# Kernel tuning notes

Measured on AMD Instinct MI355X. Metric: run time of the kernel, lower is better.

The kernel has to match this reference:

```python
import jax, jax.numpy as jnp
import numpy as np

D = 1024      # hidden_size
F = 4096      # intermediate_size
E = 16        # num_experts
TOPK = 2      # num_experts_per_tok
B, L = 1, 2048


def setup_inputs() -> dict:
    key = jax.random.key(0)
    ks = jax.random.split(key, 5)
    s = 0.02
    return {
        "x": jax.random.normal(ks[0], (B, L, D), dtype=jnp.float32),
        "gate_w": jax.random.normal(ks[1], (E, D), dtype=jnp.float32) * s,
        "w1s": jax.random.normal(ks[2], (E, F, D), dtype=jnp.float32) * s,  # per-expert w1 (out,in)
        "w2s": jax.random.normal(ks[3], (E, D, F), dtype=jnp.float32) * s,  # per-expert w2
        "w3s": jax.random.normal(ks[4], (E, F, D), dtype=jnp.float32) * s,  # per-expert w3
    }


def reference(x, gate_w, w1s, w2s, w3s):
    b, l, d = x.shape
    xf = x.reshape(-1, d)                                   # [T, D]
    router_logits = xf @ gate_w.T                           # [T, E]
    topw, topi = jax.lax.top_k(router_logits.astype(jnp.float32), TOPK)
    topw = jax.nn.softmax(topw, axis=-1).astype(x.dtype)    # [T, K]
    T = xf.shape[0]
    # dense combine weights: zero for unselected experts (same math as masked loop)
    combine = jnp.zeros((T, E), x.dtype).at[jnp.arange(T)[:, None], topi].add(topw)

    def body(acc, ew):
        w1, w2, w3, cw = ew                                 # cw: [T]
        h = jax.nn.silu(xf @ w1.T) * (xf @ w3.T)            # [T, F]
        return acc + cw[:, None] * (h @ w2.T), None

    out, _ = jax.lax.scan(body, jnp.zeros_like(xf), (w1s, w2s, w3s, combine.T))
    return out.reshape(b, l, d), router_logits
```

## Files before the change

### kernel.cpp

```cpp
#include <hip/hip_runtime.h>

#define D_DIM 1024
#define F_DIM 4096
#define E_NUM 16
#define T_NUM 2048

typedef __bf16 bf16x8 __attribute__((ext_vector_type(8)));
typedef float f32x4 __attribute__((ext_vector_type(4)));

__device__ __forceinline__ unsigned pack2bf(float a, float b) {
  unsigned ua = __builtin_bit_cast(unsigned, a);
  unsigned ub = __builtin_bit_cast(unsigned, b);
  return ((ub + 0x8000u) & 0xffff0000u) | ((ua + 0x8000u) >> 16);
}
__device__ __forceinline__ unsigned short f2bf(float a) {
  unsigned ua = __builtin_bit_cast(unsigned, a);
  return (unsigned short)((ua + 0x8000u) >> 16);
}
__device__ __forceinline__ bf16x8 cvt8(f32x4 a, f32x4 b) {
  bf16x8 r;
  r[0] = (__bf16)a[0]; r[1] = (__bf16)a[1]; r[2] = (__bf16)a[2]; r[3] = (__bf16)a[3];
  r[4] = (__bf16)b[0]; r[5] = (__bf16)b[1]; r[6] = (__bf16)b[2]; r[7] = (__bf16)b[3];
  return r;
}
__device__ __forceinline__ void gload16(const void* g, void* l) {
  __builtin_amdgcn_global_load_lds(
      (const __attribute__((address_space(1))) unsigned*)g,
      (__attribute__((address_space(3))) unsigned*)l, 16, 0, 0);
}

__global__ __launch_bounds__(256) void moe_xcast(
    const float* __restrict__ x, unsigned short* __restrict__ xbf)
{
  int i = blockIdx.x * 256 + threadIdx.x;
  const f32x4* p = (const f32x4*)x + (size_t)i * 2;
  f32x4 a = p[0], b = p[1];
  uint4 o;
  o.x = pack2bf(a[0], a[1]); o.y = pack2bf(a[2], a[3]);
  o.z = pack2bf(b[0], b[1]); o.w = pack2bf(b[2], b[3]);
  ((uint4*)xbf)[i] = o;
}

__global__ __launch_bounds__(256) void moe_router(
    const float* __restrict__ x, const float* __restrict__ gate,
    float* __restrict__ logits_out, int* __restrict__ topi, float* __restrict__ topw)
{
  __shared__ float lg[16][17];
  int tid = threadIdx.x;
  int tbase = blockIdx.x * 16;
  int tt = tid >> 4, e = tid & 15;
  const float4* xr = (const float4*)(x + (size_t)(tbase + tt) * D_DIM);
  const float4* gw = (const float4*)(gate + (size_t)e * D_DIM);
  float acc = 0.f;
  #pragma unroll 4
  for (int k = 0; k < D_DIM / 4; ++k) {
    float4 a = xr[k], b = gw[k];
    acc += a.x * b.x + a.y * b.y + a.z * b.z + a.w * b.w;
  }
  lg[tt][e] = acc;
  logits_out[(size_t)(tbase + tt) * E_NUM + e] = acc;
  __syncthreads();
  if (tid < 16) {
    int t = tid;
    float best = -1e30f; int i0 = 0;
    #pragma unroll
    for (int j = 0; j < 16; ++j) { float v = lg[t][j]; if (v > best) { best = v; i0 = j; } }
    float best1 = -1e30f; int i1 = 0;
    #pragma unroll
    for (int j = 0; j < 16; ++j) { if (j == i0) continue; float v = lg[t][j]; if (v > best1) { best1 = v; i1 = j; } }
    float e1 = __expf(best1 - best);
    float inv = 1.f / (1.f + e1);
    int gt = tbase + t;
    topi[gt * 2]     = i0;  topi[gt * 2 + 1] = i1;
    topw[gt * 2]     = inv; topw[gt * 2 + 1] = e1 * inv;
  }
}

__global__ __launch_bounds__(1024) void moe_route_build(
    const int* __restrict__ topi,
    int* __restrict__ cnt, int* __restrict__ rowbase,
    int* __restrict__ rowlist, int* __restrict__ rowpos)
{
  __shared__ int scnt[16];
  __shared__ int sbase[17];
  int wave = threadIdx.x >> 6;
  int lane = threadIdx.x & 63;
  int total = 0;
  for (int c = 0; c < (T_NUM * 2) / 64; ++c) {
    int s = c * 64 + lane;
    unsigned long long m = __ballot(topi[s] == wave);
    total += __popcll(m);
  }
  if (lane == 0) scnt[wave] = total;
  __syncthreads();
  if (threadIdx.x == 0) {
    int acc = 0;
    for (int e2 = 0; e2 < 16; ++e2) { sbase[e2] = acc; cnt[e2] = scnt[e2]; acc += scnt[e2]; }
    sbase[16] = acc;
    for (int e2 = 0; e2 <= 16; ++e2) rowbase[e2] = sbase[e2];
  }
  __syncthreads();
  int running = sbase[wave];
  for (int c = 0; c < (T_NUM * 2) / 64; ++c) {
    int s = c * 64 + lane;
    int ei = topi[s];
    unsigned long long m = __ballot(ei == wave);
    if (ei == wave) {
      int pos = running + __popcll(m & ((1ull << lane) - 1ull));
      rowlist[pos] = s;
      rowpos[s] = pos;
    }
    running += __popcll(m);
  }
}

__global__ __launch_bounds__(512, 2) void moe_gemm1(
    const unsigned short* __restrict__ xbf, const float* __restrict__ w1s, const float* __restrict__ w3s,
    const int* __restrict__ cnt, const int* __restrict__ rowbase, const int* __restrict__ rowlist,
    unsigned short* __restrict__ H)
{
  int nt = blockIdx.x, mt = blockIdx.y, e = blockIdx.z;
  int Ne = cnt[e];
  if (mt * 320 >= Ne) return;
  int rbase = rowbase[e];

  __shared__ char smem[107520];

  int tid = threadIdx.x, lane = tid & 63, wave = tid >> 6;

  const float* w1e = w1s + (size_t)e * F_DIM * D_DIM + (size_t)(nt * 128) * D_DIM;
  const float* w3e = w3s + (size_t)e * F_DIM * D_DIM + (size_t)(nt * 128) * D_DIM;
  const char* p1[2]; const char* p3[2];
  #pragma unroll
  for (int it = 0; it < 2; ++it) {
    int r = (wave * 2 + it) * 8 + (lane >> 3);
    int c = (lane & 7) ^ (r & 7);
    p1[it] = (const char*)(w1e + (size_t)r * D_DIM) + c * 16;
    p3[it] = (const char*)(w3e + (size_t)r * D_DIM) + c * 16;
  }

  const char* px[3];
  unsigned xdoff[3];
  #pragma unroll
  for (int it = 0; it < 3; ++it) {
    int ch = wave + it * 8;
    if (ch < 20) {
      int r = ch * 16 + (lane >> 2);
      int lr = mt * 320 + r;
      int tok = (lr < Ne) ? (rowlist[rbase + lr] >> 1) : 0;
      int c = (lane & 3) ^ ((r >> 1) & 3);
      px[it] = (const char*)(xbf + (size_t)tok * D_DIM) + c * 16;
      xdoff[it] = (unsigned)(ch * 1024 + lane * 16);
    } else {
      px[it] = (const char*)xbf + (lane & 3) * 16;
      xdoff[it] = 0xFFFFFFFFu;
    }
  }

  int wm = wave >> 1, wn = wave & 1;
  int lr16 = lane & 15, lq = lane >> 4;

  unsigned offA[5];
  #pragma unroll
  for (int mi = 0; mi < 5; ++mi) {
    int m = wm * 80 + mi * 16 + lr16;
    offA[mi] = (unsigned)(m * 64 + ((lq ^ ((m >> 1) & 3)) * 16));
  }
  unsigned offB[4][2];
  #pragma unroll
  for (int ni = 0; ni < 4; ++ni) {
    int n = wn * 64 + ni * 16 + lr16;
    #pragma unroll
    for (int h = 0; h < 2; ++h)
      offB[ni][h] = (unsigned)(n * 128 + (((lq * 2 + h) ^ (n & 7)) * 16));
  }

  unsigned wdst = (unsigned)((wave * 2) * 1024 + lane * 16);

  f32x4 acc1[5][4], acc3[5][4];
  #pragma unroll
  for (int i = 0; i < 5; ++i)
    #pragma unroll
    for (int j = 0; j < 4; ++j) { acc1[i][j] = {0.f,0.f,0.f,0.f}; acc3[i][j] = {0.f,0.f,0.f,0.f}; }

  auto STAGE = [&](unsigned bsel, int ks) {
    #pragma unroll
    for (int it = 0; it < 3; ++it) {
      char* dst = (xdoff[it] == 0xFFFFFFFFu)
                    ? (smem + 106496 + lane * 16)
                    : (smem + bsel * 20480u + xdoff[it]);
      gload16(px[it] + ks * 64, dst);
    }
    #pragma unroll
    for (int it = 0; it < 2; ++it) {
      gload16(p1[it] + ks * 128, smem + 40960 + bsel * 16384u + wdst + it * 1024);
      gload16(p3[it] + ks * 128, smem + 73728 + bsel * 16384u + wdst + it * 1024);
    }
  };

  STAGE(0, 0);
  unsigned buf = 0;
  for (int ks = 0; ks < 32; ++ks) {
    if (ks < 31) {
      STAGE(buf ^ 1u, ks + 1);
      asm volatile("s_waitcnt vmcnt(7)" ::: "memory");
    } else {
      asm volatile("s_waitcnt vmcnt(0)" ::: "memory");
    }
    __builtin_amdgcn_s_barrier();
    unsigned xb = buf * 20480u;
    unsigned w1b = 40960 + buf * 16384u;
    unsigned w3b = 73728 + buf * 16384u;
    bf16x8 af[5];
    #pragma unroll
    for (int mi = 0; mi < 5; ++mi)
      af[mi] = *(const bf16x8*)(smem + xb + offA[mi]);
    #pragma unroll
    for (int ni = 0; ni < 4; ++ni) {
      bf16x8 b1 = cvt8(*(const f32x4*)(smem + w1b + offB[ni][0]),
                       *(const f32x4*)(smem + w1b + offB[ni][1]));
      bf16x8 b3 = cvt8(*(const f32x4*)(smem + w3b + offB[ni][0]),
                       *(const f32x4*)(smem + w3b + offB[ni][1]));
      #pragma unroll
      for (int mi = 0; mi < 5; ++mi) {
        acc1[mi][ni] = __builtin_amdgcn_mfma_f32_16x16x32_bf16(af[mi], b1, acc1[mi][ni], 0, 0, 0);
        acc3[mi][ni] = __builtin_amdgcn_mfma_f32_16x16x32_bf16(af[mi], b3, acc3[mi][ni], 0, 0, 0);
      }
    }
    __builtin_amdgcn_s_barrier();
    buf ^= 1u;
  }

  #pragma unroll
  for (int mi = 0; mi < 5; ++mi) {
    int mb = wm * 80 + mi * 16 + lq * 4;
    #pragma unroll
    for (int r = 0; r < 4; ++r) {
      int lrow = mt * 320 + mb + r;
      if (lrow < Ne) {
        size_t hrow = (size_t)(rbase + lrow) * F_DIM;
        #pragma unroll
        for (int ni = 0; ni < 4; ++ni) {
          int f = nt * 128 + wn * 64 + ni * 16 + lr16;
          float a1v = acc1[mi][ni][r];
          float a3v = acc3[mi][ni][r];
          float hv = (a1v / (1.f + __expf(-a1v))) * a3v;
          H[hrow + f] = f2bf(hv);
        }
      }
    }
  }
}

__global__ __launch_bounds__(512, 2) void moe_gemm2(
    const unsigned short* __restrict__ H, const float* __restrict__ w2s,
    const int* __restrict__ cnt, const int* __restrict__ rowbase,
    unsigned short* __restrict__ Ybf)
{
  int nt = blockIdx.x, mt = blockIdx.y, e = blockIdx.z;
  int Ne = cnt[e];
  if (mt * 320 >= Ne) return;
  int rbase = rowbase[e];

  __shared__ char smem[114688];

  int tid = threadIdx.x, lane = tid & 63, wave = tid >> 6;

  const float* w2e = w2s + (size_t)e * D_DIM * F_DIM + (size_t)(nt * 64) * F_DIM;
  const char* pb[2];
  #pragma unroll
  for (int it = 0; it < 2; ++it) {
    int r = (wave * 2 + it) * 4 + (lane >> 4);
    int c = (lane & 15) ^ (r & 7);
    pb[it] = (const char*)(w2e + (size_t)r * F_DIM) + c * 16;
  }

  const char* pa[5];
  unsigned adoff[5];
  #pragma unroll
  for (int it = 0; it < 5; ++it) {
    int ch = wave + it * 8;
    int r = ch * 8 + (lane >> 3);
    int grow = mt * 320 + r; if (grow >= Ne) grow = Ne - 1;
    int c = (lane & 7) ^ (r & 7);
    pa[it] = (const char*)(H + (size_t)(rbase + grow) * F_DIM) + c * 16;
    adoff[it] = (unsigned)(ch * 1024 + lane * 16);
  }

  int wm = wave >> 1, wn = wave & 1;
  int lr16 = lane & 15, lq = lane >> 4;

  unsigned dstB = (unsigned)((wave * 2) * 1024 + lane * 16);

  f32x4 acc[5][2];
  #pragma unroll
  for (int i = 0; i < 5; ++i) { acc[i][0] = {0.f,0.f,0.f,0.f}; acc[i][1] = {0.f,0.f,0.f,0.f}; }

  auto STAGE = [&](unsigned bsel, int ks) {
    #pragma unroll
    for (int it = 0; it < 5; ++it)
      gload16(pa[it] + ks * 128, smem + bsel * 40960u + adoff[it]);
    #pragma unroll
    for (int it = 0; it < 2; ++it)
      gload16(pb[it] + ks * 256, smem + 81920 + bsel * 16384u + dstB + it * 1024);
  };

  STAGE(0, 0);
  unsigned buf = 0;
  for (int ks = 0; ks < 64; ++ks) {
    if (ks < 63) {
      STAGE(buf ^ 1u, ks + 1);
      asm volatile("s_waitcnt vmcnt(7)" ::: "memory");
    } else {
      asm volatile("s_waitcnt vmcnt(0)" ::: "memory");
    }
    __builtin_amdgcn_s_barrier();
    unsigned ab = buf * 40960u;
    unsigned bb = 81920 + buf * 16384u;
    #pragma unroll
    for (int ksub = 0; ksub < 2; ++ksub) {
      bf16x8 bfr[2];
      #pragma unroll
      for (int ni = 0; ni < 2; ++ni) {
        int n = wn * 32 + ni * 16 + lr16;
        unsigned o0 = (unsigned)(n * 256 + (((ksub * 8 + lq * 2 + 0) ^ (n & 7)) * 16));
        unsigned o1 = (unsigned)(n * 256 + (((ksub * 8 + lq * 2 + 1) ^ (n & 7)) * 16));
        bfr[ni] = cvt8(*(const f32x4*)(smem + bb + o0), *(const f32x4*)(smem + bb + o1));
      }
      #pragma unroll
      for (int mi = 0; mi < 5; ++mi) {
        int m = wm * 80 + mi * 16 + lr16;
        unsigned off = (unsigned)(m * 128 + (((ksub * 4 + lq) ^ (m & 7)) * 16));
        bf16x8 af = *(const bf16x8*)(smem + ab + off);
        #pragma unroll
        for (int ni = 0; ni < 2; ++ni)
          acc[mi][ni] = __builtin_amdgcn_mfma_f32_16x16x32_bf16(af, bfr[ni], acc[mi][ni], 0, 0, 0);
      }
    }
    __builtin_amdgcn_s_barrier();
    buf ^= 1u;
  }

  #pragma unroll
  for (int mi = 0; mi < 5; ++mi) {
    int mb = wm * 80 + mi * 16 + lq * 4;
    #pragma unroll
    for (int r = 0; r < 4; ++r) {
      int lrow = mt * 320 + mb + r;
      if (lrow < Ne) {
        size_t yrow = (size_t)(rbase + lrow) * D_DIM;
        #pragma unroll
        for (int ni = 0; ni < 2; ++ni) {
          int d = nt * 64 + wn * 32 + ni * 16 + lr16;
          Ybf[yrow + d] = f2bf(acc[mi][ni][r]);
        }
      }
    }
  }
}

__global__ __launch_bounds__(128) void moe_combine(
    const unsigned short* __restrict__ Ybf, const int* __restrict__ rowpos,
    const float* __restrict__ topw, float* __restrict__ out)
{
  int t = blockIdx.x, tid = threadIdx.x;
  int r0 = rowpos[t * 2], r1 = rowpos[t * 2 + 1];
  float p0 = topw[t * 2], p1 = topw[t * 2 + 1];
  uint4 a = ((const uint4*)(Ybf + (size_t)r0 * D_DIM))[tid];
  uint4 b = ((const uint4*)(Ybf + (size_t)r1 * D_DIM))[tid];
  float4 o0, o1;
  #define LO(u) __builtin_bit_cast(float, (unsigned)((u) << 16))
  #define HI(u) __builtin_bit_cast(float, (unsigned)((u) & 0xffff0000u))
  o0.x = p0 * LO(a.x) + p1 * LO(b.x);  o0.y = p0 * HI(a.x) + p1 * HI(b.x);
  o0.z = p0 * LO(a.y) + p1 * LO(b.y);  o0.w = p0 * HI(a.y) + p1 * HI(b.y);
  o1.x = p0 * LO(a.z) + p1 * LO(b.z);  o1.y = p0 * HI(a.z) + p1 * HI(b.z);
  o1.z = p0 * LO(a.w) + p1 * LO(b.w);  o1.w = p0 * HI(a.w) + p1 * HI(b.w);
  #undef LO
  #undef HI
  float4* orow = (float4*)(out + (size_t)t * D_DIM);
  orow[tid * 2]     = o0;
  orow[tid * 2 + 1] = o1;
}

extern "C" void kernel_launch(void* const* d_in, const int* in_sizes, int n_in,
                              void* d_out, int out_size, void* d_ws, size_t ws_size,
                              hipStream_t stream) {
  const float* x    = (const float*)d_in[0];
  const float* gate = (const float*)d_in[1];
  const float* w1   = (const float*)d_in[2];
  const float* w2   = (const float*)d_in[3];
  const float* w3   = (const float*)d_in[4];
  float* out    = (float*)d_out;
  float* logits = out + (size_t)T_NUM * D_DIM;

  char* ws = (char*)d_ws;
  int*   cnt     = (int*)(ws + 0);
  int*   rowbase = (int*)(ws + 64);
  int*   topi    = (int*)(ws + 1024);
  float* topw    = (float*)(ws + 1024 + 16384);
  int*   rowlist = (int*)(ws + 1024 + 32768);
  int*   rowpos  = (int*)(ws + 1024 + 49152);
  unsigned short* H   = (unsigned short*)(ws + 131072);
  unsigned short* Ybf = (unsigned short*)(ws + 131072 + 33554432);
  unsigned short* xbf = (unsigned short*)(ws + 131072 + 33554432 + 8388608);

  moe_xcast<<<(T_NUM * D_DIM) / (256 * 8), 256, 0, stream>>>(x, xbf);
  moe_router<<<T_NUM / 16, 256, 0, stream>>>(x, gate, logits, topi, topw);
  moe_route_build<<<1, 1024, 0, stream>>>(topi, cnt, rowbase, rowlist, rowpos);
  moe_gemm1<<<dim3(32, 4, 16), 512, 0, stream>>>(xbf, w1, w3, cnt, rowbase, rowlist, H);
  moe_gemm2<<<dim3(16, 4, 16), 512, 0, stream>>>(H, w2, cnt, rowbase, Ybf);
  moe_combine<<<T_NUM, 128, 0, stream>>>(Ybf, rowpos, topw, out);
}
```

Baseline: 344.4 us.

## Split MoE GEMM work across 1024-thread blocks, halving per-wave accumulators

Both expert GEMM kernels move from 512 to 1024 threads per block. In gemm1, one wave group computes the w1 projection and the other computes w3, so each wave keeps half the accumulators. The SiLU·w3 product is formed by passing the silu(w1) values through shared memory in four bands with extra barriers. In gemm2 each wave owns a single 16-wide N fragment. The grid's M dimension grows to 13 tiles so experts holding more than 1280 routed rows are covered. The aim is lower register pressure and more waves to hide latency, at the cost of extra barrier-serialised epilogue passes and one block per CU.

```diff
diff --git a/kernel.cpp b/kernel.cpp
--- a/kernel.cpp
+++ b/kernel.cpp
@@ -114,7 +114,7 @@
   }
 }
 
-__global__ __launch_bounds__(512, 2) void moe_gemm1(
+__global__ __launch_bounds__(1024, 1) void moe_gemm1(
     const unsigned short* __restrict__ xbf, const float* __restrict__ w1s, const float* __restrict__ w3s,
     const int* __restrict__ cnt, const int* __restrict__ rowbase, const int* __restrict__ rowlist,
     unsigned short* __restrict__ H)
@@ -124,40 +124,39 @@
   if (mt * 320 >= Ne) return;
   int rbase = rowbase[e];
 
-  __shared__ char smem[107520];
+  __shared__ char smem[106496];
 
   int tid = threadIdx.x, lane = tid & 63, wave = tid >> 6;
+
+  int nx = (wave < 4) ? 2 : 1;
+  const char* px[2];
+  unsigned xoff[2];
+  #pragma unroll
+  for (int it = 0; it < 2; ++it) {
+    int ch = wave + it * 16;
+    if (ch < 20) {
+      int row = ch * 16 + (lane >> 2);
+      int lr = mt * 320 + row;
+      int tok = (lr < Ne) ? (rowlist[rbase + lr] >> 1) : 0;
+      int c4 = (lane & 3) ^ ((row >> 1) & 3);
+      px[it] = (const char*)(xbf + (size_t)tok * D_DIM) + c4 * 16;
+      xoff[it] = (unsigned)(ch * 1024 + lane * 16);
+    } else {
+      px[it] = (const char*)xbf;
+      xoff[it] = 0;
+    }
+  }
 
   const float* w1e = w1s + (size_t)e * F_DIM * D_DIM + (size_t)(nt * 128) * D_DIM;
   const float* w3e = w3s + (size_t)e * F_DIM * D_DIM + (size_t)(nt * 128) * D_DIM;
-  const char* p1[2]; const char* p3[2];
-  #pragma unroll
-  for (int it = 0; it < 2; ++it) {
-    int r = (wave * 2 + it) * 8 + (lane >> 3);
-    int c = (lane & 7) ^ (r & 7);
-    p1[it] = (const char*)(w1e + (size_t)r * D_DIM) + c * 16;
-    p3[it] = (const char*)(w3e + (size_t)r * D_DIM) + c * 16;
-  }
-
-  const char* px[3];
-  unsigned xdoff[3];
-  #pragma unroll
-  for (int it = 0; it < 3; ++it) {
-    int ch = wave + it * 8;
-    if (ch < 20) {
-      int r = ch * 16 + (lane >> 2);
-      int lr = mt * 320 + r;
-      int tok = (lr < Ne) ? (rowlist[rbase + lr] >> 1) : 0;
-      int c = (lane & 3) ^ ((r >> 1) & 3);
-      px[it] = (const char*)(xbf + (size_t)tok * D_DIM) + c * 16;
-      xdoff[it] = (unsigned)(ch * 1024 + lane * 16);
-    } else {
-      px[it] = (const char*)xbf + (lane & 3) * 16;
-      xdoff[it] = 0xFFFFFFFFu;
-    }
-  }
-
-  int wm = wave >> 1, wn = wave & 1;
+  int rw = wave * 8 + (lane >> 3);
+  int cw = (lane & 7) ^ (rw & 7);
+  const char* pw1 = (const char*)(w1e + (size_t)rw * D_DIM) + cw * 16;
+  const char* pw3 = (const char*)(w3e + (size_t)rw * D_DIM) + cw * 16;
+  unsigned woff = (unsigned)(wave * 1024 + lane * 16);
+
+  int wgrp = wave >> 3, wl = wave & 7;
+  int wm = wl >> 1, wn = wl & 1;
   int lr16 = lane & 15, lq = lane >> 4;
 
   unsigned offA[5];
@@ -168,34 +167,25 @@
   }
   unsigned offB[4][2];
   #pragma unroll
-  for (int ni = 0; ni < 4; ++ni) {
-    int n = wn * 64 + ni * 16 + lr16;
+  for (int nf = 0; nf < 4; ++nf) {
+    int n = wn * 64 + nf * 16 + lr16;
     #pragma unroll
     for (int h = 0; h < 2; ++h)
-      offB[ni][h] = (unsigned)(n * 128 + (((lq * 2 + h) ^ (n & 7)) * 16));
-  }
-
-  unsigned wdst = (unsigned)((wave * 2) * 1024 + lane * 16);
-
-  f32x4 acc1[5][4], acc3[5][4];
+      offB[nf][h] = (unsigned)(n * 128 + (((lq * 2 + h) ^ (n & 7)) * 16));
+  }
+  unsigned wbase0 = wgrp ? 73728u : 40960u;
+
+  f32x4 acc[5][4];
   #pragma unroll
   for (int i = 0; i < 5; ++i)
     #pragma unroll
-    for (int j = 0; j < 4; ++j) { acc1[i][j] = {0.f,0.f,0.f,0.f}; acc3[i][j] = {0.f,0.f,0.f,0.f}; }
+    for (int j = 0; j < 4; ++j) acc[i][j] = {0.f, 0.f, 0.f, 0.f};
 
   auto STAGE = [&](unsigned bsel, int ks) {
-    #pragma unroll
-    for (int it = 0; it < 3; ++it) {
-      char* dst = (xdoff[it] == 0xFFFFFFFFu)
-                    ? (smem + 106496 + lane * 16)
-                    : (smem + bsel * 20480u + xdoff[it]);
-      gload16(px[it] + ks * 64, dst);
-    }
-    #pragma unroll
-    for (int it = 0; it < 2; ++it) {
-      gload16(p1[it] + ks * 128, smem + 40960 + bsel * 16384u + wdst + it * 1024);
-      gload16(p3[it] + ks * 128, smem + 73728 + bsel * 16384u + wdst + it * 1024);
-    }
+    gload16(px[0] + ks * 64, smem + bsel * 20480u + xoff[0]);
+    if (nx == 2) gload16(px[1] + ks * 64, smem + bsel * 20480u + xoff[1]);
+    gload16(pw1 + ks * 128, smem + 40960 + bsel * 16384u + woff);
+    gload16(pw3 + ks * 128, smem + 73728 + bsel * 16384u + woff);
   };
 
   STAGE(0, 0);
@@ -203,56 +193,72 @@
   for (int ks = 0; ks < 32; ++ks) {
     if (ks < 31) {
       STAGE(buf ^ 1u, ks + 1);
-      asm volatile("s_waitcnt vmcnt(7)" ::: "memory");
+      if (wave < 4) asm volatile("s_waitcnt vmcnt(4)" ::: "memory");
+      else          asm volatile("s_waitcnt vmcnt(3)" ::: "memory");
     } else {
       asm volatile("s_waitcnt vmcnt(0)" ::: "memory");
     }
     __builtin_amdgcn_s_barrier();
     unsigned xb = buf * 20480u;
-    unsigned w1b = 40960 + buf * 16384u;
-    unsigned w3b = 73728 + buf * 16384u;
-    bf16x8 af[5];
-    #pragma unroll
-    for (int mi = 0; mi < 5; ++mi)
-      af[mi] = *(const bf16x8*)(smem + xb + offA[mi]);
-    #pragma unroll
-    for (int ni = 0; ni < 4; ++ni) {
-      bf16x8 b1 = cvt8(*(const f32x4*)(smem + w1b + offB[ni][0]),
-                       *(const f32x4*)(smem + w1b + offB[ni][1]));
-      bf16x8 b3 = cvt8(*(const f32x4*)(smem + w3b + offB[ni][0]),
-                       *(const f32x4*)(smem + w3b + offB[ni][1]));
+    unsigned wb = wbase0 + buf * 16384u;
+    bf16x8 bfr[4];
+    #pragma unroll
+    for (int nf = 0; nf < 4; ++nf)
+      bfr[nf] = cvt8(*(const f32x4*)(smem + wb + offB[nf][0]),
+                     *(const f32x4*)(smem + wb + offB[nf][1]));
+    #pragma unroll
+    for (int mi = 0; mi < 5; ++mi) {
+      bf16x8 af = *(const bf16x8*)(smem + xb + offA[mi]);
+      #pragma unroll
+      for (int nf = 0; nf < 4; ++nf)
+        acc[mi][nf] = __builtin_amdgcn_mfma_f32_16x16x32_bf16(af, bfr[nf], acc[mi][nf], 0, 0, 0);
+    }
+    __builtin_amdgcn_s_barrier();
+    buf ^= 1u;
+  }
+
+  float* xch = (float*)smem;
+  for (int band = 0; band < 4; ++band) {
+    if (wgrp == 0 && wm == band) {
       #pragma unroll
       for (int mi = 0; mi < 5; ++mi) {
-        acc1[mi][ni] = __builtin_amdgcn_mfma_f32_16x16x32_bf16(af[mi], b1, acc1[mi][ni], 0, 0, 0);
-        acc3[mi][ni] = __builtin_amdgcn_mfma_f32_16x16x32_bf16(af[mi], b3, acc3[mi][ni], 0, 0, 0);
-      }
-    }
-    __builtin_amdgcn_s_barrier();
-    buf ^= 1u;
-  }
-
-  #pragma unroll
-  for (int mi = 0; mi < 5; ++mi) {
-    int mb = wm * 80 + mi * 16 + lq * 4;
-    #pragma unroll
-    for (int r = 0; r < 4; ++r) {
-      int lrow = mt * 320 + mb + r;
-      if (lrow < Ne) {
-        size_t hrow = (size_t)(rbase + lrow) * F_DIM;
         #pragma unroll
-        for (int ni = 0; ni < 4; ++ni) {
-          int f = nt * 128 + wn * 64 + ni * 16 + lr16;
-          float a1v = acc1[mi][ni][r];
-          float a3v = acc3[mi][ni][r];
-          float hv = (a1v / (1.f + __expf(-a1v))) * a3v;
-          H[hrow + f] = f2bf(hv);
+        for (int r = 0; r < 4; ++r) {
+          int rb = mi * 16 + lq * 4 + r;
+          #pragma unroll
+          for (int nf = 0; nf < 4; ++nf) {
+            int col = wn * 64 + nf * 16 + lr16;
+            float a = acc[mi][nf][r];
+            xch[rb * 132 + col] = a / (1.f + __expf(-a));
+          }
         }
       }
     }
-  }
-}
-
-__global__ __launch_bounds__(512, 2) void moe_gemm2(
+    asm volatile("s_waitcnt lgkmcnt(0)" ::: "memory");
+    __builtin_amdgcn_s_barrier();
+    if (wgrp == 1 && wm == band) {
+      #pragma unroll
+      for (int mi = 0; mi < 5; ++mi) {
+        #pragma unroll
+        for (int r = 0; r < 4; ++r) {
+          int rb = mi * 16 + lq * 4 + r;
+          int lrow = mt * 320 + band * 80 + rb;
+          if (lrow < Ne) {
+            size_t hrow = (size_t)(rbase + lrow) * F_DIM;
+            #pragma unroll
+            for (int nf = 0; nf < 4; ++nf) {
+              int col = wn * 64 + nf * 16 + lr16;
+              H[hrow + nt * 128 + col] = f2bf(xch[rb * 132 + col] * acc[mi][nf][r]);
+            }
+          }
+        }
+      }
+    }
+    __builtin_amdgcn_s_barrier();
+  }
+}
+
+__global__ __launch_bounds__(1024, 1) void moe_gemm2(
     const unsigned short* __restrict__ H, const float* __restrict__ w2s,
     const int* __restrict__ cnt, const int* __restrict__ rowbase,
     unsigned short* __restrict__ Ybf)
@@ -266,43 +272,43 @@
 
   int tid = threadIdx.x, lane = tid & 63, wave = tid >> 6;
 
+  int na = (wave < 8) ? 3 : 2;
+  const char* pa[3];
+  unsigned aoff[3];
+  #pragma unroll
+  for (int it = 0; it < 3; ++it) {
+    int ch = wave + it * 16;
+    if (ch < 40) {
+      int row = ch * 8 + (lane >> 3);
+      int grow = mt * 320 + row; if (grow >= Ne) grow = Ne - 1;
+      int c8 = (lane & 7) ^ (row & 7);
+      pa[it] = (const char*)(H + (size_t)(rbase + grow) * F_DIM) + c8 * 16;
+      aoff[it] = (unsigned)(ch * 1024 + lane * 16);
+    } else {
+      pa[it] = (const char*)H;
+      aoff[it] = 0;
+    }
+  }
+
   const float* w2e = w2s + (size_t)e * D_DIM * F_DIM + (size_t)(nt * 64) * F_DIM;
-  const char* pb[2];
-  #pragma unroll
-  for (int it = 0; it < 2; ++it) {
-    int r = (wave * 2 + it) * 4 + (lane >> 4);
-    int c = (lane & 15) ^ (r & 7);
-    pb[it] = (const char*)(w2e + (size_t)r * F_DIM) + c * 16;
-  }
-
-  const char* pa[5];
-  unsigned adoff[5];
-  #pragma unroll
-  for (int it = 0; it < 5; ++it) {
-    int ch = wave + it * 8;
-    int r = ch * 8 + (lane >> 3);
-    int grow = mt * 320 + r; if (grow >= Ne) grow = Ne - 1;
-    int c = (lane & 7) ^ (r & 7);
-    pa[it] = (const char*)(H + (size_t)(rbase + grow) * F_DIM) + c * 16;
-    adoff[it] = (unsigned)(ch * 1024 + lane * 16);
-  }
-
-  int wm = wave >> 1, wn = wave & 1;
+  int rw = wave * 4 + (lane >> 4);
+  int cw = (lane & 15) ^ (rw & 7);
+  const char* pw2 = (const char*)(w2e + (size_t)rw * F_DIM) + cw * 16;
+  unsigned woff = (unsigned)(wave * 1024 + lane * 16);
+
+  int wm = wave >> 2, wn = wave & 3;
   int lr16 = lane & 15, lq = lane >> 4;
-
-  unsigned dstB = (unsigned)((wave * 2) * 1024 + lane * 16);
-
-  f32x4 acc[5][2];
-  #pragma unroll
-  for (int i = 0; i < 5; ++i) { acc[i][0] = {0.f,0.f,0.f,0.f}; acc[i][1] = {0.f,0.f,0.f,0.f}; }
+  int n = wn * 16 + lr16;
+
+  f32x4 acc[5];
+  #pragma unroll
+  for (int i = 0; i < 5; ++i) acc[i] = {0.f, 0.f, 0.f, 0.f};
 
   auto STAGE = [&](unsigned bsel, int ks) {
-    #pragma unroll
-    for (int it = 0; it < 5; ++it)
-      gload16(pa[it] + ks * 128, smem + bsel * 40960u + adoff[it]);
-    #pragma unroll
-    for (int it = 0; it < 2; ++it)
-      gload16(pb[it] + ks * 256, smem + 81920 + bsel * 16384u + dstB + it * 1024);
+    gload16(pa[0] + ks * 128, smem + bsel * 40960u + aoff[0]);
+    gload16(pa[1] + ks * 128, smem + bsel * 40960u + aoff[1]);
+    if (na == 3) gload16(pa[2] + ks * 128, smem + bsel * 40960u + aoff[2]);
+    gload16(pw2 + ks * 256, smem + 81920 + bsel * 16384u + woff);
   };
 
   STAGE(0, 0);
@@ -310,7 +316,8 @@
   for (int ks = 0; ks < 64; ++ks) {
     if (ks < 63) {
       STAGE(buf ^ 1u, ks + 1);
-      asm volatile("s_waitcnt vmcnt(7)" ::: "memory");
+      if (wave < 8) asm volatile("s_waitcnt vmcnt(4)" ::: "memory");
+      else          asm volatile("s_waitcnt vmcnt(3)" ::: "memory");
     } else {
       asm volatile("s_waitcnt vmcnt(0)" ::: "memory");
     }
@@ -319,22 +326,15 @@
     unsigned bb = 81920 + buf * 16384u;
     #pragma unroll
     for (int ksub = 0; ksub < 2; ++ksub) {
-      bf16x8 bfr[2];
-      #pragma unroll
-      for (int ni = 0; ni < 2; ++ni) {
-        int n = wn * 32 + ni * 16 + lr16;
-        unsigned o0 = (unsigned)(n * 256 + (((ksub * 8 + lq * 2 + 0) ^ (n & 7)) * 16));
-        unsigned o1 = (unsigned)(n * 256 + (((ksub * 8 + lq * 2 + 1) ^ (n & 7)) * 16));
-        bfr[ni] = cvt8(*(const f32x4*)(smem + bb + o0), *(const f32x4*)(smem + bb + o1));
-      }
+      unsigned o0 = (unsigned)(n * 256 + (((ksub * 8 + lq * 2 + 0) ^ (n & 7)) * 16));
+      unsigned o1 = (unsigned)(n * 256 + (((ksub * 8 + lq * 2 + 1) ^ (n & 7)) * 16));
+      bf16x8 bfr = cvt8(*(const f32x4*)(smem + bb + o0), *(const f32x4*)(smem + bb + o1));
       #pragma unroll
       for (int mi = 0; mi < 5; ++mi) {
         int m = wm * 80 + mi * 16 + lr16;
         unsigned off = (unsigned)(m * 128 + (((ksub * 4 + lq) ^ (m & 7)) * 16));
         bf16x8 af = *(const bf16x8*)(smem + ab + off);
-        #pragma unroll
-        for (int ni = 0; ni < 2; ++ni)
-          acc[mi][ni] = __builtin_amdgcn_mfma_f32_16x16x32_bf16(af, bfr[ni], acc[mi][ni], 0, 0, 0);
+        acc[mi] = __builtin_amdgcn_mfma_f32_16x16x32_bf16(af, bfr, acc[mi], 0, 0, 0);
       }
     }
     __builtin_amdgcn_s_barrier();
@@ -349,11 +349,7 @@
       int lrow = mt * 320 + mb + r;
       if (lrow < Ne) {
         size_t yrow = (size_t)(rbase + lrow) * D_DIM;
-        #pragma unroll
-        for (int ni = 0; ni < 2; ++ni) {
-          int d = nt * 64 + wn * 32 + ni * 16 + lr16;
-          Ybf[yrow + d] = f2bf(acc[mi][ni][r]);
-        }
+        Ybf[yrow + nt * 64 + n] = f2bf(acc[mi][r]);
       }
     }
   }
@@ -407,7 +403,7 @@
   moe_xcast<<<(T_NUM * D_DIM) / (256 * 8), 256, 0, stream>>>(x, xbf);
   moe_router<<<T_NUM / 16, 256, 0, stream>>>(x, gate, logits, topi, topw);
   moe_route_build<<<1, 1024, 0, stream>>>(topi, cnt, rowbase, rowlist, rowpos);
-  moe_gemm1<<<dim3(32, 4, 16), 512, 0, stream>>>(xbf, w1, w3, cnt, rowbase, rowlist, H);
-  moe_gemm2<<<dim3(16, 4, 16), 512, 0, stream>>>(H, w2, cnt, rowbase, Ybf);
+  moe_gemm1<<<dim3(32, 13, 16), 1024, 0, stream>>>(xbf, w1, w3, cnt, rowbase, rowlist, H);
+  moe_gemm2<<<dim3(16, 13, 16), 1024, 0, stream>>>(H, w2, cnt, rowbase, Ybf);
   moe_combine<<<T_NUM, 128, 0, stream>>>(Ybf, rowpos, topw, out);
 }
```

Result: slower. 470.7 us (+36.7%).

## Pre-gather routed tokens to bf16 and widen gemm2 N tile

Applied to the files above, without the earlier changes.

A new gather kernel replaces the full-x bf16 cast and writes each routed token's row contiguously in expert order. gemm1 can then load activations with plain strided addressing instead of per-row token lookups, and it no longer needs the dummy-destination path for idle waves. gemm2 doubles its output-column tile from 64 to 128, so each H tile is reused across more columns and fewer H loads are issued. The M grid is cut to two 320-row tiles per expert, which caps each expert at 640 tokens; gemm2's larger LDS footprint may also reduce occupancy.

```diff
diff --git a/kernel.cpp b/kernel.cpp
--- a/kernel.cpp
+++ b/kernel.cpp
@@ -27,18 +27,6 @@
   __builtin_amdgcn_global_load_lds(
       (const __attribute__((address_space(1))) unsigned*)g,
       (__attribute__((address_space(3))) unsigned*)l, 16, 0, 0);
-}
-
-__global__ __launch_bounds__(256) void moe_xcast(
-    const float* __restrict__ x, unsigned short* __restrict__ xbf)
-{
-  int i = blockIdx.x * 256 + threadIdx.x;
-  const f32x4* p = (const f32x4*)x + (size_t)i * 2;
-  f32x4 a = p[0], b = p[1];
-  uint4 o;
-  o.x = pack2bf(a[0], a[1]); o.y = pack2bf(a[2], a[3]);
-  o.z = pack2bf(b[0], b[1]); o.w = pack2bf(b[2], b[3]);
-  ((uint4*)xbf)[i] = o;
 }
 
 __global__ __launch_bounds__(256) void moe_router(
@@ -114,9 +102,21 @@
   }
 }
 
+__global__ __launch_bounds__(256) void moe_gather(
+    const float* __restrict__ x, const int* __restrict__ rowlist,
+    const int* __restrict__ rowbase, unsigned short* __restrict__ xg)
+{
+  int pos = blockIdx.x;
+  int total = rowbase[16];
+  int tok = (pos < total) ? (rowlist[pos] >> 1) : 0;
+  f32x4 v = ((const f32x4*)(x + (size_t)tok * D_DIM))[threadIdx.x];
+  ((uint2*)(xg + (size_t)pos * D_DIM))[threadIdx.x] =
+      make_uint2(pack2bf(v[0], v[1]), pack2bf(v[2], v[3]));
+}
+
 __global__ __launch_bounds__(512, 2) void moe_gemm1(
-    const unsigned short* __restrict__ xbf, const float* __restrict__ w1s, const float* __restrict__ w3s,
-    const int* __restrict__ cnt, const int* __restrict__ rowbase, const int* __restrict__ rowlist,
+    const unsigned short* __restrict__ xg, const float* __restrict__ w1s, const float* __restrict__ w3s,
+    const int* __restrict__ cnt, const int* __restrict__ rowbase,
     unsigned short* __restrict__ H)
 {
   int nt = blockIdx.x, mt = blockIdx.y, e = blockIdx.z;
@@ -124,9 +124,25 @@
   if (mt * 320 >= Ne) return;
   int rbase = rowbase[e];
 
-  __shared__ char smem[107520];
+  __shared__ char smem[106496];
 
   int tid = threadIdx.x, lane = tid & 63, wave = tid >> 6;
+
+  const char* px[3];
+  unsigned xoff[3];
+  #pragma unroll
+  for (int it = 0; it < 3; ++it) {
+    int ch = wave + it * 8;
+    if (ch < 20) {
+      int row = ch * 16 + (lane >> 2);
+      int slot = (lane & 3) ^ ((row >> 1) & 3);
+      px[it] = (const char*)(xg + (size_t)(rbase + mt * 320 + row) * D_DIM) + slot * 16;
+      xoff[it] = (unsigned)(ch * 1024 + lane * 16);
+    } else {
+      px[it] = (const char*)xg;
+      xoff[it] = 0;
+    }
+  }
 
   const float* w1e = w1s + (size_t)e * F_DIM * D_DIM + (size_t)(nt * 128) * D_DIM;
   const float* w3e = w3s + (size_t)e * F_DIM * D_DIM + (size_t)(nt * 128) * D_DIM;
@@ -139,24 +155,6 @@
     p3[it] = (const char*)(w3e + (size_t)r * D_DIM) + c * 16;
   }
 
-  const char* px[3];
-  unsigned xdoff[3];
-  #pragma unroll
-  for (int it = 0; it < 3; ++it) {
-    int ch = wave + it * 8;
-    if (ch < 20) {
-      int r = ch * 16 + (lane >> 2);
-      int lr = mt * 320 + r;
-      int tok = (lr < Ne) ? (rowlist[rbase + lr] >> 1) : 0;
-      int c = (lane & 3) ^ ((r >> 1) & 3);
-      px[it] = (const char*)(xbf + (size_t)tok * D_DIM) + c * 16;
-      xdoff[it] = (unsigned)(ch * 1024 + lane * 16);
-    } else {
-      px[it] = (const char*)xbf + (lane & 3) * 16;
-      xdoff[it] = 0xFFFFFFFFu;
-    }
-  }
-
   int wm = wave >> 1, wn = wave & 1;
   int lr16 = lane & 15, lq = lane >> 4;
 
@@ -184,13 +182,9 @@
     for (int j = 0; j < 4; ++j) { acc1[i][j] = {0.f,0.f,0.f,0.f}; acc3[i][j] = {0.f,0.f,0.f,0.f}; }
 
   auto STAGE = [&](unsigned bsel, int ks) {
-    #pragma unroll
-    for (int it = 0; it < 3; ++it) {
-      char* dst = (xdoff[it] == 0xFFFFFFFFu)
-                    ? (smem + 106496 + lane * 16)
-                    : (smem + bsel * 20480u + xdoff[it]);
-      gload16(px[it] + ks * 64, dst);
-    }
+    gload16(px[0] + ks * 64, smem + bsel * 20480u + xoff[0]);
+    gload16(px[1] + ks * 64, smem + bsel * 20480u + xoff[1]);
+    if (wave < 4) gload16(px[2] + ks * 64, smem + bsel * 20480u + xoff[2]);
     #pragma unroll
     for (int it = 0; it < 2; ++it) {
       gload16(p1[it] + ks * 128, smem + 40960 + bsel * 16384u + wdst + it * 1024);
@@ -203,7 +197,8 @@
   for (int ks = 0; ks < 32; ++ks) {
     if (ks < 31) {
       STAGE(buf ^ 1u, ks + 1);
-      asm volatile("s_waitcnt vmcnt(7)" ::: "memory");
+      if (wave < 4) asm volatile("s_waitcnt vmcnt(7)" ::: "memory");
+      else          asm volatile("s_waitcnt vmcnt(6)" ::: "memory");
     } else {
       asm volatile("s_waitcnt vmcnt(0)" ::: "memory");
     }
@@ -262,47 +257,59 @@
   if (mt * 320 >= Ne) return;
   int rbase = rowbase[e];
 
-  __shared__ char smem[114688];
+  __shared__ char smem[147456];
 
   int tid = threadIdx.x, lane = tid & 63, wave = tid >> 6;
 
-  const float* w2e = w2s + (size_t)e * D_DIM * F_DIM + (size_t)(nt * 64) * F_DIM;
-  const char* pb[2];
-  #pragma unroll
-  for (int it = 0; it < 2; ++it) {
-    int r = (wave * 2 + it) * 4 + (lane >> 4);
-    int c = (lane & 15) ^ (r & 7);
-    pb[it] = (const char*)(w2e + (size_t)r * F_DIM) + c * 16;
-  }
-
   const char* pa[5];
-  unsigned adoff[5];
+  unsigned aoff[5];
   #pragma unroll
   for (int it = 0; it < 5; ++it) {
     int ch = wave + it * 8;
-    int r = ch * 8 + (lane >> 3);
-    int grow = mt * 320 + r; if (grow >= Ne) grow = Ne - 1;
-    int c = (lane & 7) ^ (r & 7);
-    pa[it] = (const char*)(H + (size_t)(rbase + grow) * F_DIM) + c * 16;
-    adoff[it] = (unsigned)(ch * 1024 + lane * 16);
+    int row = ch * 8 + (lane >> 3);
+    int grow = mt * 320 + row; if (grow >= Ne) grow = Ne - 1;
+    int c8 = (lane & 7) ^ (row & 7);
+    pa[it] = (const char*)(H + (size_t)(rbase + grow) * F_DIM) + c8 * 16;
+    aoff[it] = (unsigned)(ch * 1024 + lane * 16);
+  }
+
+  const float* w2e = w2s + (size_t)e * D_DIM * F_DIM + (size_t)(nt * 128) * F_DIM;
+  const char* pb[4];
+  unsigned boff[4];
+  #pragma unroll
+  for (int it = 0; it < 4; ++it) {
+    int ch = wave + it * 8;
+    int row = ch * 4 + (lane >> 4);
+    int c = (lane & 15) ^ (row & 7);
+    pb[it] = (const char*)(w2e + (size_t)row * F_DIM) + c * 16;
+    boff[it] = (unsigned)(ch * 1024 + lane * 16);
   }
 
   int wm = wave >> 1, wn = wave & 1;
   int lr16 = lane & 15, lq = lane >> 4;
 
-  unsigned dstB = (unsigned)((wave * 2) * 1024 + lane * 16);
-
-  f32x4 acc[5][2];
-  #pragma unroll
-  for (int i = 0; i < 5; ++i) { acc[i][0] = {0.f,0.f,0.f,0.f}; acc[i][1] = {0.f,0.f,0.f,0.f}; }
+  unsigned offB[4][2];
+  #pragma unroll
+  for (int ni = 0; ni < 4; ++ni) {
+    int n = wn * 64 + ni * 16 + lr16;
+    #pragma unroll
+    for (int h = 0; h < 2; ++h)
+      offB[ni][h] = (unsigned)(n * 256 + (((lq * 2 + h) ^ (n & 7)) * 16));
+  }
+
+  f32x4 acc[5][4];
+  #pragma unroll
+  for (int i = 0; i < 5; ++i)
+    #pragma unroll
+    for (int j = 0; j < 4; ++j) acc[i][j] = {0.f, 0.f, 0.f, 0.f};
 
   auto STAGE = [&](unsigned bsel, int ks) {
     #pragma unroll
     for (int it = 0; it < 5; ++it)
-      gload16(pa[it] + ks * 128, smem + bsel * 40960u + adoff[it]);
-    #pragma unroll
-    for (int it = 0; it < 2; ++it)
-      gload16(pb[it] + ks * 256, smem + 81920 + bsel * 16384u + dstB + it * 1024);
+      gload16(pa[it] + ks * 128, smem + bsel * 40960u + aoff[it]);
+    #pragma unroll
+    for (int it = 0; it < 4; ++it)
+      gload16(pb[it] + ks * 256, smem + 81920 + bsel * 32768u + boff[it]);
   };
 
   STAGE(0, 0);
@@ -310,19 +317,19 @@
   for (int ks = 0; ks < 64; ++ks) {
     if (ks < 63) {
       STAGE(buf ^ 1u, ks + 1);
-      asm volatile("s_waitcnt vmcnt(7)" ::: "memory");
+      asm volatile("s_waitcnt vmcnt(9)" ::: "memory");
     } else {
       asm volatile("s_waitcnt vmcnt(0)" ::: "memory");
     }
     __builtin_amdgcn_s_barrier();
     unsigned ab = buf * 40960u;
-    unsigned bb = 81920 + buf * 16384u;
+    unsigned bb = 81920 + buf * 32768u;
     #pragma unroll
     for (int ksub = 0; ksub < 2; ++ksub) {
-      bf16x8 bfr[2];
+      bf16x8 bfr[4];
       #pragma unroll
-      for (int ni = 0; ni < 2; ++ni) {
-        int n = wn * 32 + ni * 16 + lr16;
+      for (int ni = 0; ni < 4; ++ni) {
+        int n = wn * 64 + ni * 16 + lr16;
         unsigned o0 = (unsigned)(n * 256 + (((ksub * 8 + lq * 2 + 0) ^ (n & 7)) * 16));
         unsigned o1 = (unsigned)(n * 256 + (((ksub * 8 + lq * 2 + 1) ^ (n & 7)) * 16));
         bfr[ni] = cvt8(*(const f32x4*)(smem + bb + o0), *(const f32x4*)(smem + bb + o1));
@@ -333,7 +340,7 @@
         unsigned off = (unsigned)(m * 128 + (((ksub * 4 + lq) ^ (m & 7)) * 16));
         bf16x8 af = *(const bf16x8*)(smem + ab + off);
         #pragma unroll
-        for (int ni = 0; ni < 2; ++ni)
+        for (int ni = 0; ni < 4; ++ni)
           acc[mi][ni] = __builtin_amdgcn_mfma_f32_16x16x32_bf16(af, bfr[ni], acc[mi][ni], 0, 0, 0);
       }
     }
@@ -350,8 +357,8 @@
       if (lrow < Ne) {
         size_t yrow = (size_t)(rbase + lrow) * D_DIM;
         #pragma unroll
-        for (int ni = 0; ni < 2; ++ni) {
-          int d = nt * 64 + wn * 32 + ni * 16 + lr16;
+        for (int ni = 0; ni < 4; ++ni) {
+          int d = nt * 128 + wn * 64 + ni * 16 + lr16;
           Ybf[yrow + d] = f2bf(acc[mi][ni][r]);
         }
       }
@@ -400,14 +407,14 @@
   float* topw    = (float*)(ws + 1024 + 16384);
   int*   rowlist = (int*)(ws + 1024 + 32768);
   int*   rowpos  = (int*)(ws + 1024 + 49152);
-  unsigned short* H   = (unsigned short*)(ws + 131072);
-  unsigned short* Ybf = (unsigned short*)(ws + 131072 + 33554432);
-  unsigned short* xbf = (unsigned short*)(ws + 131072 + 33554432 + 8388608);
-
-  moe_xcast<<<(T_NUM * D_DIM) / (256 * 8), 256, 0, stream>>>(x, xbf);
+  unsigned short* H  = (unsigned short*)(ws + 131072);
+  unsigned short* xg  = (unsigned short*)(ws + 131072 + 33554432);
+  unsigned short* Ybf = xg;
+
   moe_router<<<T_NUM / 16, 256, 0, stream>>>(x, gate, logits, topi, topw);
   moe_route_build<<<1, 1024, 0, stream>>>(topi, cnt, rowbase, rowlist, rowpos);
-  moe_gemm1<<<dim3(32, 4, 16), 512, 0, stream>>>(xbf, w1, w3, cnt, rowbase, rowlist, H);
-  moe_gemm2<<<dim3(16, 4, 16), 512, 0, stream>>>(H, w2, cnt, rowbase, Ybf);
+  moe_gather<<<6144, 256, 0, stream>>>(x, rowlist, rowbase, xg);
+  moe_gemm1<<<dim3(32, 2, 16), 512, 0, stream>>>(xg, w1, w3, cnt, rowbase, H);
+  moe_gemm2<<<dim3(8, 2, 16), 512, 0, stream>>>(H, w2, cnt, rowbase, Ybf);
   moe_combine<<<T_NUM, 128, 0, stream>>>(Ybf, rowpos, topw, out);
 }
```

New measurement: 346.3 us. About the same (+0.5%).
